# Optimization experiments

Measured on AMD Instinct MI355X. Metric: run time of the kernel, lower is better.

Reference implementation:

```python
import jax, jax.numpy as jnp
import numpy as np

B = 16384
D = 256        # feature_dim
EPS = 1e-5     # BatchNorm eps
NUM_CLASSES = 26

# cross-attention index pattern from the original double loop:
# for i in range(4): for j in range(4): if j != i: kv = features[4 - j - 1], q = features[i]
_Q_IDX = np.array([i for i in range(4) for j in range(4) if j != i])
_KV_IDX = np.array([3 - j for i in range(4) for j in range(4) if j != i])


def setup_inputs() -> dict:
    key = jax.random.key(0)
    ks = jax.random.split(key, 32)
    def n(k, shape, s=0.02):
        return jax.random.normal(k, shape, dtype=jnp.float32) * s
    inp = {
        'x_context': jax.random.normal(ks[0], (B, 2048), jnp.float32),
        'x_body':    jax.random.normal(ks[1], (B, 1024), jnp.float32),
        'x_face':    jax.random.normal(ks[2], (B, 512), jnp.float32),
        'x_text':    jax.random.normal(ks[3], (B, 768), jnp.float32),
        # modality input projections
        'w_ctx':  n(ks[4], (D, 2048)), 'b_ctx':  n(ks[5], (D,)),
        'w_body': n(ks[6], (D, 1024)), 'b_body': n(ks[7], (D,)),
        'w_face': n(ks[8], (D, 512)),  'b_face': n(ks[9], (D,)),
        'w_text': n(ks[10], (D, 768)), 'b_text': n(ks[11], (D,)),
        # shared nn.MultiheadAttention params (in_proj packs q,k,v)
        'in_proj_w': n(ks[12], (3 * D, D)), 'in_proj_b': n(ks[13], (3 * D,)),
        'out_w': n(ks[14], (D, D)), 'out_b': n(ks[15], (D,)),
        # gate MLP
        'gate_w1': n(ks[16], (D, D)), 'gate_b1': n(ks[17], (D,)),
        'gate_w2': n(ks[18], (1, D)), 'gate_b2': n(ks[19], (1,)),
        # head
        'fc1_w': n(ks[20], (D, D)), 'fc1_b': n(ks[21], (D,)),
        'bn_g': jnp.ones((D,), jnp.float32), 'bn_b': jnp.zeros((D,), jnp.float32),
        'fc2_w': n(ks[22], (NUM_CLASSES, D)), 'fc2_b': n(ks[23], (NUM_CLASSES,)),
    }
    return inp


def reference(x_context, x_body, x_face, x_text,
              w_ctx, b_ctx, w_body, b_body, w_face, b_face, w_text, b_text,
              in_proj_w, in_proj_b, out_w, out_b,
              gate_w1, gate_b1, gate_w2, gate_b2,
              fc1_w, fc1_b, bn_g, bn_b, fc2_w, fc2_b):
    # per-modality projections -> (4, B, D)
    f = jnp.stack([
        x_context @ w_ctx.T + b_ctx,
        x_body @ w_body.T + b_body,
        x_face @ w_face.T + b_face,
        x_text @ w_text.T + b_text,
    ], axis=0)

    # nn.MultiheadAttention with a single key/value token: softmax over one
    # logit is identically 1 (zero grad to q/k projections), so
    # attn(q, kv) = out_proj(v_proj(kv)) exactly.
    w_v = in_proj_w[2 * D:]
    b_v = in_proj_b[2 * D:]
    A = (f @ w_v.T + b_v) @ out_w.T + out_b            # (4, B, D)

    # self attention: attended_i + query_i, then mean over 4 modalities
    feats_self = jnp.mean(A + f, axis=0)               # (B, D)
    # cross attention: 12 (query, kv) pairs, then mean over 12
    feats_cross = jnp.mean(A[_KV_IDX] + f[_Q_IDX], axis=0)  # (B, D)

    gate = jax.nn.sigmoid(
        jax.nn.relu(feats_self @ gate_w1.T + gate_b1) @ gate_w2.T + gate_b2
    )                                                   # (B, 1)
    combined = gate * feats_self + (1.0 - gate) * feats_cross

    h = combined @ fc1_w.T + fc1_b
    # BatchNorm1d, training-mode batch statistics (biased var, as torch)
    mu = jnp.mean(h, axis=0)
    var = jnp.var(h, axis=0)
    h = (h - mu) * jax.lax.rsqrt(var + EPS) * bn_g + bn_b
    h = jax.nn.relu(h)
    # dropout omitted (deterministic reference)
    return h @ fc2_w.T + fc2_b                          # (B, 26)
```

## Files before the change

### kernel.cpp

```cpp
#include <hip/hip_runtime.h>
#include <hip/hip_bf16.h>
#include <stdint.h>

#define DM    256
#define KC    4352
#define NCLS  26

typedef __bf16 bf16;
typedef __attribute__((ext_vector_type(8))) __bf16 bf16x8;
typedef __attribute__((ext_vector_type(4))) __bf16 bf16x4;
typedef __attribute__((ext_vector_type(4))) float f32x4;
typedef __attribute__((ext_vector_type(4))) int i32x4;
typedef __attribute__((ext_vector_type(2))) int i32x2;

#define WQ_OFF    0u
#define SW_OFF    1114112u
#define COLF_OFF  1115136u
#define BSUM4_OFF 1116160u
#define CS_OFF    1117184u
#define CQ_OFF    1118208u
#define PTBF_OFF  1119232u
#define CC_OFF    1250304u
#define GT_OFF    1251328u
#define G_OFF     1382400u
#define FC2P_OFF  1383424u
#define FBAR_OFF  1400832u
#define H_OFF     9789440u

__device__ __forceinline__ bf16x8 cvt8(float4 a, float4 b) {
  bf16x8 r;
  r[0] = (bf16)a.x; r[1] = (bf16)a.y; r[2] = (bf16)a.z; r[3] = (bf16)a.w;
  r[4] = (bf16)b.x; r[5] = (bf16)b.y; r[6] = (bf16)b.z; r[7] = (bf16)b.w;
  return r;
}

__device__ __forceinline__ void gld_lds16(const void* g, void* l) {
  __builtin_amdgcn_global_load_lds(
      (const __attribute__((address_space(1))) void*)g,
      (__attribute__((address_space(3))) void*)l, 16, 0, 0);
}

__device__ __forceinline__ const float* pick(const float* x0, const float* x1,
                                             const float* x2, const float* x3,
                                             int k0, int& L, int& ko) {
  if (k0 < 2048)      { L = 2048; ko = k0;        return x0; }
  else if (k0 < 3072) { L = 1024; ko = k0 - 2048; return x1; }
  else if (k0 < 3584) { L = 512;  ko = k0 - 3072; return x2; }
  else                { L = 768;  ko = k0 - 3584; return x3; }
}

__device__ __forceinline__ int qpack4(float4 v, float s) {
  int a = (int)rintf(fminf(fmaxf(v.x * s, -127.f), 127.f));
  int b = (int)rintf(fminf(fmaxf(v.y * s, -127.f), 127.f));
  int c = (int)rintf(fminf(fmaxf(v.z * s, -127.f), 127.f));
  int d = (int)rintf(fminf(fmaxf(v.w * s, -127.f), 127.f));
  return (a & 255) | ((b & 255) << 8) | ((c & 255) << 16) | ((d & 255) << 24);
}

#define SXQ 25.4f

__global__ __launch_bounds__(256) void k_sw(
    const float* __restrict__ w0, const float* __restrict__ w1,
    const float* __restrict__ w2, const float* __restrict__ w3,
    float* __restrict__ sw) {
  __shared__ float red[4];
  int c = blockIdx.x, t = threadIdx.x;
  float m = 0.f;
  for (int k = t * 4; k < 2048; k += 1024) {
    float4 v = *(const float4*)(w0 + c * 2048 + k);
    m = fmaxf(m, fmaxf(fmaxf(fabsf(v.x), fabsf(v.y)), fmaxf(fabsf(v.z), fabsf(v.w))));
  }
  if (t * 4 < 1024) {
    float4 v = *(const float4*)(w1 + c * 1024 + t * 4);
    m = fmaxf(m, fmaxf(fmaxf(fabsf(v.x), fabsf(v.y)), fmaxf(fabsf(v.z), fabsf(v.w))));
  }
  if (t * 4 < 512) {
    float4 v = *(const float4*)(w2 + c * 512 + t * 4);
    m = fmaxf(m, fmaxf(fmaxf(fabsf(v.x), fabsf(v.y)), fmaxf(fabsf(v.z), fabsf(v.w))));
  }
  if (t * 4 < 768) {
    float4 v = *(const float4*)(w3 + c * 768 + t * 4);
    m = fmaxf(m, fmaxf(fmaxf(fabsf(v.x), fabsf(v.y)), fmaxf(fabsf(v.z), fabsf(v.w))));
  }
#pragma unroll
  for (int off = 32; off; off >>= 1) m = fmaxf(m, __shfl_xor(m, off));
  if ((t & 63) == 0) red[t >> 6] = m;
  __syncthreads();
  if (t == 0) sw[c] = fmaxf(fmaxf(red[0], red[1]), fmaxf(red[2], red[3]));
}

__global__ __launch_bounds__(256) void k_preA(
    const float* __restrict__ w0, const float* __restrict__ w1,
    const float* __restrict__ w2, const float* __restrict__ w3,
    const float* __restrict__ b0, const float* __restrict__ b1,
    const float* __restrict__ b2, const float* __restrict__ b3,
    const float* __restrict__ fc2_w, const float* __restrict__ sw,
    char* __restrict__ Wq, float* __restrict__ colf, float* __restrict__ bsum4,
    float* __restrict__ cs, float* __restrict__ cq, bf16* __restrict__ fc2p) {
  int bid = blockIdx.x;
  if (bid < 272) {
    int u = bid * 256 + threadIdx.x;
    int n16 = u / 4352;
    int rem = u % 4352;
    int kt = rem >> 6, lane = rem & 63;
    int col = n16 * 16 + (lane & 15);
    int k = kt * 64 + (lane >> 4) * 16;
    const float* src; int o;
    if (k < 2048)      { src = w0 + col * 2048; o = k; }
    else if (k < 3072) { src = w1 + col * 1024; o = k - 2048; }
    else if (k < 3584) { src = w2 + col * 512;  o = k - 3072; }
    else               { src = w3 + col * 768;  o = k - 3584; }
    float s = 127.f / sw[col];
    float4 a = *(const float4*)(src + o);
    float4 b = *(const float4*)(src + o + 4);
    float4 c = *(const float4*)(src + o + 8);
    float4 d = *(const float4*)(src + o + 12);
    i32x4 q;
    q[0] = qpack4(a, s); q[1] = qpack4(b, s); q[2] = qpack4(c, s); q[3] = qpack4(d, s);
    *(i32x4*)(Wq + (size_t)u * 16) = q;
  } else {
    int d = threadIdx.x;
    bsum4[d] = 0.25f * (b0[d] + b1[d] + b2[d] + b3[d]);
    colf[d] = 0.25f * (5.f / 127.f) * (sw[d] / 127.f);
    cs[d] = 0.f; cq[d] = 0.f;
#pragma unroll
    for (int rep = 0; rep < 4; ++rep) {
      int u2 = rep * 256 + threadIdx.x;
      int n16 = u2 >> 9, kf = (u2 >> 6) & 7, lane = u2 & 63;
      int row = n16 * 16 + (lane & 15);
      int kk = kf * 32 + (lane >> 4) * 8;
      bf16x8 v = {};
      if (row < 26) {
        float4 a = *(const float4*)(fc2_w + row * 256 + kk);
        float4 b = *(const float4*)(fc2_w + row * 256 + kk + 4);
        v = cvt8(a, b);
      }
      *(bf16x8*)(fc2p + (size_t)u2 * 8) = v;
    }
  }
}

__global__ __launch_bounds__(256) void k_preB(
    const float* __restrict__ in_proj_w, const float* __restrict__ in_proj_b,
    const float* __restrict__ out_w, const float* __restrict__ out_b,
    bf16* __restrict__ PTbf, float* __restrict__ cc) {
  int o0 = blockIdx.x * 16;
  int tid = threadIdx.x;
  int os = tid >> 6, iq = tid & 63;
  f32x4 facc[4] = {};
  float cacc[4] = {0.f, 0.f, 0.f, 0.f};
  for (int j = 0; j < 256; ++j) {
    f32x4 v = *(const f32x4*)(in_proj_w + (size_t)(512 + j) * 256 + iq * 4);
    float bv = in_proj_b[512 + j];
#pragma unroll
    for (int oo = 0; oo < 4; ++oo) {
      float w = out_w[(o0 + os * 4 + oo) * 256 + j];
      facc[oo] += v * w;
      cacc[oo] += bv * w;
    }
  }
#pragma unroll
  for (int oo = 0; oo < 4; ++oo) {
    int o = o0 + os * 4 + oo;
    bf16x4 r;
    r[0] = (bf16)facc[oo][0]; r[1] = (bf16)facc[oo][1];
    r[2] = (bf16)facc[oo][2]; r[3] = (bf16)facc[oo][3];
    *(bf16x4*)(PTbf + (size_t)o * 256 + iq * 4) = r;
    if (iq == 0) cc[o] = cacc[oo] + out_b[o];
  }
}

__global__ __launch_bounds__(256) void k_preC(
    const bf16* __restrict__ PTbf, const float* __restrict__ cc,
    const float* __restrict__ fc1_w, const float* __restrict__ fc1_b,
    bf16* __restrict__ GT, float* __restrict__ g) {
  __shared__ float fc1s[256];
  __shared__ float part[4][256];
  __shared__ float gbuf[256];
  int j = blockIdx.x;
  int tid = threadIdx.x;
  fc1s[tid] = fc1_w[j * 256 + tid];
  __syncthreads();
  int os = tid >> 6, lane = tid & 63;
  float a8[8] = {};
  for (int it = 0; it < 32; ++it) {
    int o = os * 64 + it * 2 + (lane >> 5);
    bf16x8 p = *(const bf16x8*)(PTbf + (size_t)o * 256 + (lane & 31) * 8);
    float w = fc1s[o];
#pragma unroll
    for (int e = 0; e < 8; ++e) a8[e] += (float)p[e] * w;
  }
#pragma unroll
  for (int e = 0; e < 8; ++e) a8[e] += __shfl_xor(a8[e], 32);
  if (lane < 32) {
#pragma unroll
    for (int e = 0; e < 8; ++e) part[os][(lane & 31) * 8 + e] = a8[e];
  }
  gbuf[tid] = cc[tid] * fc1s[tid];
  __syncthreads();
  int i = tid;
  float s = fc1s[i] + part[0][i] + part[1][i] + part[2][i] + part[3][i];
  int is = (i & ~63) | ((((i >> 3) & 7) ^ (j & 7)) << 3) | (i & 7);
  GT[j * 256 + is] = (bf16)s;
  if (tid == 0) {
    float t = 0.f;
    for (int o = 0; o < 256; ++o) t += gbuf[o];
    g[j] = t + fc1_b[j];
  }
}

__global__ __launch_bounds__(512, 2) void k_gemm1(
    const float* __restrict__ x0, const float* __restrict__ x1,
    const float* __restrict__ x2, const float* __restrict__ x3,
    const char* __restrict__ Wq, const float* __restrict__ colf,
    const float* __restrict__ bsum4, bf16* __restrict__ fbar) {
  __shared__ __align__(16) char ldsA[3][8192];
  int mt = blockIdx.x;
  int tid = threadIdx.x;
  int lane = tid & 63, wid = tid >> 6;
  int fr = lane & 15, fq = lane >> 4;
  i32x4 acc[4][2] = {};

  int arow = tid >> 3, achk = tid & 7;
  int wa = arow * 128 + (achk >> 2) * 64 + (((achk & 3) ^ (arow & 3)) << 4);
  const size_t xrow = (size_t)(mt * 64 + arow);
  const char* wq = Wq + (size_t)lane * 16;

  float4 arA[4], arB[4];
  i32x4 bbA[2][2], bbB[2][2];

  {
    int L, ko; const float* xs = pick(x0, x1, x2, x3, 0, L, ko);
    const float4* ap = (const float4*)(xs + xrow * L + ko) + achk * 4;
    float4 t0 = ap[0], t1 = ap[1], t2 = ap[2], t3 = ap[3];
#pragma unroll
    for (int n = 0; n < 2; ++n)
#pragma unroll
      for (int sb = 0; sb < 2; ++sb)
        bbA[n][sb] = *(const i32x4*)(wq + ((size_t)((2 * wid + n) * 68 + sb) << 10));
    xs = pick(x0, x1, x2, x3, 128, L, ko);
    ap = (const float4*)(xs + xrow * L + ko) + achk * 4;
    arB[0] = ap[0]; arB[1] = ap[1]; arB[2] = ap[2]; arB[3] = ap[3];
    i32x4 q;
    q[0] = qpack4(t0, SXQ); q[1] = qpack4(t1, SXQ);
    q[2] = qpack4(t2, SXQ); q[3] = qpack4(t3, SXQ);
    *(i32x4*)(&ldsA[0][wa]) = q;
    __builtin_amdgcn_sched_barrier(0);
    asm volatile("s_waitcnt lgkmcnt(0)" ::: "memory");
    __builtin_amdgcn_s_barrier();
    __builtin_amdgcn_sched_barrier(0);
  }

#define K1_BODY(S, BBU, BBL, ARU, ARL)                                         \
  do {                                                                         \
    int s1 = (s0 == 2) ? 0 : s0 + 1;                                           \
    if ((S) < 33) {                                                            \
      _Pragma("unroll") for (int n = 0; n < 2; ++n)                            \
      _Pragma("unroll") for (int sb = 0; sb < 2; ++sb)                         \
        BBL[n][sb] = *(const i32x4*)(wq +                                      \
            ((size_t)((2 * wid + n) * 68 + 2 * ((S) + 1) + sb) << 10));        \
    }                                                                          \
    if ((S) < 32) {                                                            \
      int L_, ko_;                                                             \
      const float* xs_ = pick(x0, x1, x2, x3, ((S) + 2) * 128, L_, ko_);       \
      const float4* ap_ = (const float4*)(xs_ + xrow * L_ + ko_) + achk * 4;   \
      ARL[0] = ap_[0]; ARL[1] = ap_[1]; ARL[2] = ap_[2]; ARL[3] = ap_[3];      \
    }                                                                          \
    if ((S) < 33) {                                                            \
      i32x4 q_;                                                                \
      q_[0] = qpack4(ARU[0], SXQ); q_[1] = qpack4(ARU[1], SXQ);                \
      q_[2] = qpack4(ARU[2], SXQ); q_[3] = qpack4(ARU[3], SXQ);                \
      *(i32x4*)(&ldsA[s1][wa]) = q_;                                           \
    }                                                                          \
    __builtin_amdgcn_sched_barrier(0);                                         \
    asm volatile("s_waitcnt lgkmcnt(0)" ::: "memory");                         \
    __builtin_amdgcn_s_barrier();                                              \
    __builtin_amdgcn_sched_barrier(0);                                         \
    const char* A_ = &ldsA[s0][0];                                             \
    i32x4 av[4][2];                                                            \
    _Pragma("unroll") for (int m = 0; m < 4; ++m) {                            \
      int row_ = m * 16 + fr;                                                  \
      _Pragma("unroll") for (int sb = 0; sb < 2; ++sb)                         \
        av[m][sb] = *(const i32x4*)(A_ + row_ * 128 + sb * 64 +                \
                                    ((fq ^ (row_ & 3)) << 4));                 \
    }                                                                          \
    __builtin_amdgcn_s_setprio(1);                                             \
    _Pragma("unroll") for (int sb = 0; sb < 2; ++sb)                           \
    _Pragma("unroll") for (int m = 0; m < 4; ++m)                              \
    _Pragma("unroll") for (int n = 0; n < 2; ++n)                              \
      acc[m][n] = __builtin_amdgcn_mfma_i32_16x16x64_i8(                       \
          av[m][sb], BBU[n][sb], acc[m][n], 0, 0, 0);                          \
    __builtin_amdgcn_s_setprio(0);                                             \
    s0 = s1;                                                                   \
  } while (0)

  int s0 = 0;
  for (int ss = 0; ss < 17; ++ss) {
    int S0 = ss * 2;
    K1_BODY(S0,     bbA, bbB, arB, arA);
    K1_BODY(S0 + 1, bbB, bbA, arA, arB);
  }
#undef K1_BODY

#pragma unroll
  for (int n = 0; n < 2; ++n) {
    int col = (2 * wid + n) * 16 + fr;
    float cf = colf[col];
    float b4 = bsum4[col];
#pragma unroll
    for (int m = 0; m < 4; ++m) {
      int row0 = mt * 64 + m * 16 + fq * 4;
#pragma unroll
      for (int r = 0; r < 4; ++r) {
        int row = row0 + r;
        int csw = (col & ~63) | ((((col >> 3) & 7) ^ (row & 7)) << 3) | (col & 7);
        fbar[(size_t)row * DM + csw] = (bf16)((float)acc[m][n][r] * cf + b4);
      }
    }
  }
}

__global__ __launch_bounds__(256, 4) void k_gemm2(
    const bf16* __restrict__ fbar, const bf16* __restrict__ GT,
    const float* __restrict__ g, bf16* __restrict__ h,
    float* __restrict__ cs, float* __restrict__ cq) {
  __shared__ __align__(16) bf16 lds[2][8192];
  int bid = blockIdx.x;
  int tile = (bid & 7) * 128 + (bid >> 3);
  int mt = tile >> 2, nt = tile & 3;
  int tid = threadIdx.x;
  int lane = tid & 63, wid = tid >> 6;
  int wr = wid >> 1, wc = wid & 1;
  int fr = lane & 15, fq = lane >> 4;
  f32x4 acc[2][2] = {};

  const size_t arow0 = (size_t)(mt * 64 + (tid >> 3)) * DM + (tid & 7) * 8;
  const size_t arow1 = (size_t)(mt * 64 + 32 + (tid >> 3)) * DM + (tid & 7) * 8;
  const size_t grow0 = (size_t)(nt * 64 + (tid >> 3)) * DM + (tid & 7) * 8;
  const size_t grow1 = (size_t)(nt * 64 + 32 + (tid >> 3)) * DM + (tid & 7) * 8;

  gld_lds16(fbar + arow0, &lds[0][tid * 8]);
  gld_lds16(fbar + arow1, &lds[0][2048 + tid * 8]);
  gld_lds16(GT + grow0, &lds[0][4096 + tid * 8]);
  gld_lds16(GT + grow1, &lds[0][4096 + 2048 + tid * 8]);
  __syncthreads();

  for (int kt = 0; kt < 4; ++kt) {
    int cur = kt & 1;
    if (kt < 3) {
      int k0 = (kt + 1) * 64;
      gld_lds16(fbar + arow0 + k0, &lds[cur ^ 1][tid * 8]);
      gld_lds16(fbar + arow1 + k0, &lds[cur ^ 1][2048 + tid * 8]);
      gld_lds16(GT + grow0 + k0, &lds[cur ^ 1][4096 + tid * 8]);
      gld_lds16(GT + grow1 + k0, &lds[cur ^ 1][4096 + 2048 + tid * 8]);
    }
    const bf16* A  = &lds[cur][0];
    const bf16* Bb = &lds[cur][4096];
    bf16x8 av[2][2], bv[2][2];
#pragma unroll
    for (int m = 0; m < 2; ++m) {
      int row = wr * 32 + m * 16 + fr;
#pragma unroll
      for (int kk = 0; kk < 2; ++kk)
        av[m][kk] = *(const bf16x8*)(A + row * 64 + ((((kk << 2) | fq) ^ (row & 7)) << 3));
    }
#pragma unroll
    for (int n = 0; n < 2; ++n) {
      int row = wc * 32 + n * 16 + fr;
#pragma unroll
      for (int kk = 0; kk < 2; ++kk)
        bv[n][kk] = *(const bf16x8*)(Bb + row * 64 + ((((kk << 2) | fq) ^ (row & 7)) << 3));
    }
#pragma unroll
    for (int kk = 0; kk < 2; ++kk)
#pragma unroll
      for (int m = 0; m < 2; ++m)
#pragma unroll
        for (int n = 0; n < 2; ++n)
          acc[m][n] = __builtin_amdgcn_mfma_f32_16x16x32_bf16(av[m][kk], bv[n][kk], acc[m][n], 0, 0, 0);
    __syncthreads();
  }

#pragma unroll
  for (int n = 0; n < 2; ++n) {
    int col = nt * 64 + wc * 32 + n * 16 + fr;
    float gv = g[col];
    float s = 0.f, q = 0.f;
#pragma unroll
    for (int m = 0; m < 2; ++m) {
      int row0 = mt * 64 + wr * 32 + m * 16 + fq * 4;
#pragma unroll
      for (int r = 0; r < 4; ++r) {
        float v = acc[m][n][r] + gv;
        h[(size_t)(row0 + r) * DM + col] = (bf16)v;
        s += v; q += v * v;
      }
    }
    s += __shfl_xor(s, 16); s += __shfl_xor(s, 32);
    q += __shfl_xor(q, 16); q += __shfl_xor(q, 32);
    if (fq == 0) { atomicAdd(&cs[col], s); atomicAdd(&cq[col], q); }
  }
}

__global__ __launch_bounds__(512) void k_fc2(
    const bf16* __restrict__ h, const float* __restrict__ cs, const float* __restrict__ cq,
    const float* __restrict__ bn_g, const float* __restrict__ bn_b,
    const bf16* __restrict__ fc2p, const float* __restrict__ fc2_b,
    float* __restrict__ out) {
  __shared__ float sdtd[512];
  int tid = threadIdx.x;
  int lane = tid & 63, wid = tid >> 6;
  int fr = lane & 15, fq = lane >> 4;
  if (tid < 256) {
    float mu = cs[tid] * (1.f / 16384.f);
    float var = cq[tid] * (1.f / 16384.f) - mu * mu;
    float s = bn_g[tid] * rsqrtf(var + 1e-5f);
    sdtd[tid] = s;
    sdtd[256 + tid] = bn_b[tid] - mu * s;
  }
  __syncthreads();
  int mtile = wid >> 1, n16 = wid & 1;
  int row0 = blockIdx.x * 64 + mtile * 16;
  f32x4 acc = {};
#pragma unroll
  for (int kf = 0; kf < 8; ++kf) {
    int c0 = kf * 32 + fq * 8;
    bf16x8 hv = *(const bf16x8*)(h + (size_t)(row0 + fr) * 256 + c0);
    bf16x8 y;
#pragma unroll
    for (int e = 0; e < 8; ++e) {
      float v = (float)hv[e] * sdtd[c0 + e] + sdtd[256 + c0 + e];
      y[e] = (bf16)fmaxf(v, 0.f);
    }
    bf16x8 bv = *(const bf16x8*)(fc2p + ((size_t)(n16 * 8 + kf) << 9) + lane * 8);
    acc = __builtin_amdgcn_mfma_f32_16x16x32_bf16(y, bv, acc, 0, 0, 0);
  }
  int col = n16 * 16 + fr;
  if (col < NCLS) {
    float bb = fc2_b[col];
#pragma unroll
    for (int r = 0; r < 4; ++r)
      out[(size_t)(row0 + fq * 4 + r) * NCLS + col] = acc[r] + bb;
  }
}

extern "C" void kernel_launch(void* const* d_in, const int* in_sizes, int n_in,
                              void* d_out, int out_size, void* d_ws, size_t ws_size,
                              hipStream_t stream) {
  (void)in_sizes; (void)n_in; (void)out_size; (void)ws_size;
  const float* x0 = (const float*)d_in[0];
  const float* x1 = (const float*)d_in[1];
  const float* x2 = (const float*)d_in[2];
  const float* x3 = (const float*)d_in[3];
  const float* w0 = (const float*)d_in[4];
  const float* b0 = (const float*)d_in[5];
  const float* w1 = (const float*)d_in[6];
  const float* b1 = (const float*)d_in[7];
  const float* w2 = (const float*)d_in[8];
  const float* b2 = (const float*)d_in[9];
  const float* w3 = (const float*)d_in[10];
  const float* b3 = (const float*)d_in[11];
  const float* in_proj_w = (const float*)d_in[12];
  const float* in_proj_b = (const float*)d_in[13];
  const float* out_w = (const float*)d_in[14];
  const float* out_b = (const float*)d_in[15];
  const float* fc1_w = (const float*)d_in[20];
  const float* fc1_b = (const float*)d_in[21];
  const float* bn_g = (const float*)d_in[22];
  const float* bn_b = (const float*)d_in[23];
  const float* fc2_w = (const float*)d_in[24];
  const float* fc2_b = (const float*)d_in[25];

  char* ws = (char*)d_ws;
  char* Wq    = ws + WQ_OFF;
  float* sw   = (float*)(ws + SW_OFF);
  float* colf = (float*)(ws + COLF_OFF);
  float* bsum4= (float*)(ws + BSUM4_OFF);
  float* cs   = (float*)(ws + CS_OFF);
  float* cq   = (float*)(ws + CQ_OFF);
  bf16* PTbf  = (bf16*)(ws + PTBF_OFF);
  float* cc   = (float*)(ws + CC_OFF);
  bf16* GT    = (bf16*)(ws + GT_OFF);
  float* g    = (float*)(ws + G_OFF);
  bf16* fc2p  = (bf16*)(ws + FC2P_OFF);
  bf16* fbar  = (bf16*)(ws + FBAR_OFF);
  bf16* h     = (bf16*)(ws + H_OFF);
  float* out  = (float*)d_out;

  k_sw<<<dim3(256), dim3(256), 0, stream>>>(w0, w1, w2, w3, sw);
  k_preA<<<dim3(273), dim3(256), 0, stream>>>(w0, w1, w2, w3, b0, b1, b2, b3,
                                              fc2_w, sw, Wq, colf, bsum4, cs, cq, fc2p);
  k_preB<<<dim3(16), dim3(256), 0, stream>>>(in_proj_w, in_proj_b, out_w, out_b, PTbf, cc);
  k_preC<<<dim3(256), dim3(256), 0, stream>>>(PTbf, cc, fc1_w, fc1_b, GT, g);
  k_gemm1<<<dim3(256), dim3(512), 0, stream>>>(x0, x1, x2, x3, Wq, colf, bsum4, fbar);
  k_gemm2<<<dim3(1024), dim3(256), 0, stream>>>(fbar, GT, g, h, cs, cq);
  k_fc2<<<dim3(256), dim3(512), 0, stream>>>(h, cs, cq, bn_g, bn_b, fc2p, fc2_b, out);
}
```

Baseline: 130.6 us.

## Fuse second GEMM into first GEMM epilogue and merge preB into sw kernel

The second GEMM (fbar times GT) now runs inside k_gemm1's epilogue. The fbar tile stays in LDS, and the B operand is read straight from a fragment-packed GT layout in global memory, so the fbar round-trip to HBM and the k_gemm2 launch both go away. The small preB weight-folding kernel is merged into the sw kernel as extra blocks, saving one more launch. The cost is 32KB more LDS per gemm1 block, which may cut occupancy, and each block now computes a full 64x256 tile on its own, so there is less parallelism than the old 1024-block gemm2.

```diff
diff --git a/kernel.cpp b/kernel.cpp
--- a/kernel.cpp
+++ b/kernel.cpp
@@ -11,7 +11,6 @@
 typedef __attribute__((ext_vector_type(4))) __bf16 bf16x4;
 typedef __attribute__((ext_vector_type(4))) float f32x4;
 typedef __attribute__((ext_vector_type(4))) int i32x4;
-typedef __attribute__((ext_vector_type(2))) int i32x2;
 
 #define WQ_OFF    0u
 #define SW_OFF    1114112u
@@ -24,20 +23,13 @@
 #define GT_OFF    1251328u
 #define G_OFF     1382400u
 #define FC2P_OFF  1383424u
-#define FBAR_OFF  1400832u
-#define H_OFF     9789440u
+#define H_OFF     1400832u
 
 __device__ __forceinline__ bf16x8 cvt8(float4 a, float4 b) {
   bf16x8 r;
   r[0] = (bf16)a.x; r[1] = (bf16)a.y; r[2] = (bf16)a.z; r[3] = (bf16)a.w;
   r[4] = (bf16)b.x; r[5] = (bf16)b.y; r[6] = (bf16)b.z; r[7] = (bf16)b.w;
   return r;
-}
-
-__device__ __forceinline__ void gld_lds16(const void* g, void* l) {
-  __builtin_amdgcn_global_load_lds(
-      (const __attribute__((address_space(1))) void*)g,
-      (__attribute__((address_space(3))) void*)l, 16, 0, 0);
 }
 
 __device__ __forceinline__ const float* pick(const float* x0, const float* x1,
@@ -59,34 +51,63 @@
 
 #define SXQ 25.4f
 
-__global__ __launch_bounds__(256) void k_sw(
+__global__ __launch_bounds__(256) void k_swB(
     const float* __restrict__ w0, const float* __restrict__ w1,
     const float* __restrict__ w2, const float* __restrict__ w3,
-    float* __restrict__ sw) {
-  __shared__ float red[4];
-  int c = blockIdx.x, t = threadIdx.x;
-  float m = 0.f;
-  for (int k = t * 4; k < 2048; k += 1024) {
-    float4 v = *(const float4*)(w0 + c * 2048 + k);
-    m = fmaxf(m, fmaxf(fmaxf(fabsf(v.x), fabsf(v.y)), fmaxf(fabsf(v.z), fabsf(v.w))));
-  }
-  if (t * 4 < 1024) {
-    float4 v = *(const float4*)(w1 + c * 1024 + t * 4);
-    m = fmaxf(m, fmaxf(fmaxf(fabsf(v.x), fabsf(v.y)), fmaxf(fabsf(v.z), fabsf(v.w))));
-  }
-  if (t * 4 < 512) {
-    float4 v = *(const float4*)(w2 + c * 512 + t * 4);
-    m = fmaxf(m, fmaxf(fmaxf(fabsf(v.x), fabsf(v.y)), fmaxf(fabsf(v.z), fabsf(v.w))));
-  }
-  if (t * 4 < 768) {
-    float4 v = *(const float4*)(w3 + c * 768 + t * 4);
-    m = fmaxf(m, fmaxf(fmaxf(fabsf(v.x), fabsf(v.y)), fmaxf(fabsf(v.z), fabsf(v.w))));
-  }
-#pragma unroll
-  for (int off = 32; off; off >>= 1) m = fmaxf(m, __shfl_xor(m, off));
-  if ((t & 63) == 0) red[t >> 6] = m;
-  __syncthreads();
-  if (t == 0) sw[c] = fmaxf(fmaxf(red[0], red[1]), fmaxf(red[2], red[3]));
+    const float* __restrict__ in_proj_w, const float* __restrict__ in_proj_b,
+    const float* __restrict__ out_w, const float* __restrict__ out_b,
+    float* __restrict__ sw, bf16* __restrict__ PTbf, float* __restrict__ cc) {
+  if (blockIdx.x < 256) {
+    __shared__ float red[4];
+    int c = blockIdx.x, t = threadIdx.x;
+    float m = 0.f;
+    for (int k = t * 4; k < 2048; k += 1024) {
+      float4 v = *(const float4*)(w0 + c * 2048 + k);
+      m = fmaxf(m, fmaxf(fmaxf(fabsf(v.x), fabsf(v.y)), fmaxf(fabsf(v.z), fabsf(v.w))));
+    }
+    if (t * 4 < 1024) {
+      float4 v = *(const float4*)(w1 + c * 1024 + t * 4);
+      m = fmaxf(m, fmaxf(fmaxf(fabsf(v.x), fabsf(v.y)), fmaxf(fabsf(v.z), fabsf(v.w))));
+    }
+    if (t * 4 < 512) {
+      float4 v = *(const float4*)(w2 + c * 512 + t * 4);
+      m = fmaxf(m, fmaxf(fmaxf(fabsf(v.x), fabsf(v.y)), fmaxf(fabsf(v.z), fabsf(v.w))));
+    }
+    if (t * 4 < 768) {
+      float4 v = *(const float4*)(w3 + c * 768 + t * 4);
+      m = fmaxf(m, fmaxf(fmaxf(fabsf(v.x), fabsf(v.y)), fmaxf(fabsf(v.z), fabsf(v.w))));
+    }
+#pragma unroll
+    for (int off = 32; off; off >>= 1) m = fmaxf(m, __shfl_xor(m, off));
+    if ((t & 63) == 0) red[t >> 6] = m;
+    __syncthreads();
+    if (t == 0) sw[c] = fmaxf(fmaxf(red[0], red[1]), fmaxf(red[2], red[3]));
+  } else {
+    int o0 = (blockIdx.x - 256) * 16;
+    int tid = threadIdx.x;
+    int os = tid >> 6, iq = tid & 63;
+    f32x4 facc[4] = {};
+    float cacc[4] = {0.f, 0.f, 0.f, 0.f};
+    for (int j = 0; j < 256; ++j) {
+      f32x4 v = *(const f32x4*)(in_proj_w + (size_t)(512 + j) * 256 + iq * 4);
+      float bv = in_proj_b[512 + j];
+#pragma unroll
+      for (int oo = 0; oo < 4; ++oo) {
+        float w = out_w[(o0 + os * 4 + oo) * 256 + j];
+        facc[oo] += v * w;
+        cacc[oo] += bv * w;
+      }
+    }
+#pragma unroll
+    for (int oo = 0; oo < 4; ++oo) {
+      int o = o0 + os * 4 + oo;
+      bf16x4 r;
+      r[0] = (bf16)facc[oo][0]; r[1] = (bf16)facc[oo][1];
+      r[2] = (bf16)facc[oo][2]; r[3] = (bf16)facc[oo][3];
+      *(bf16x4*)(PTbf + (size_t)o * 256 + iq * 4) = r;
+      if (iq == 0) cc[o] = cacc[oo] + out_b[o];
+    }
+  }
 }
 
 __global__ __launch_bounds__(256) void k_preA(
@@ -140,40 +161,10 @@
   }
 }
 
-__global__ __launch_bounds__(256) void k_preB(
-    const float* __restrict__ in_proj_w, const float* __restrict__ in_proj_b,
-    const float* __restrict__ out_w, const float* __restrict__ out_b,
-    bf16* __restrict__ PTbf, float* __restrict__ cc) {
-  int o0 = blockIdx.x * 16;
-  int tid = threadIdx.x;
-  int os = tid >> 6, iq = tid & 63;
-  f32x4 facc[4] = {};
-  float cacc[4] = {0.f, 0.f, 0.f, 0.f};
-  for (int j = 0; j < 256; ++j) {
-    f32x4 v = *(const f32x4*)(in_proj_w + (size_t)(512 + j) * 256 + iq * 4);
-    float bv = in_proj_b[512 + j];
-#pragma unroll
-    for (int oo = 0; oo < 4; ++oo) {
-      float w = out_w[(o0 + os * 4 + oo) * 256 + j];
-      facc[oo] += v * w;
-      cacc[oo] += bv * w;
-    }
-  }
-#pragma unroll
-  for (int oo = 0; oo < 4; ++oo) {
-    int o = o0 + os * 4 + oo;
-    bf16x4 r;
-    r[0] = (bf16)facc[oo][0]; r[1] = (bf16)facc[oo][1];
-    r[2] = (bf16)facc[oo][2]; r[3] = (bf16)facc[oo][3];
-    *(bf16x4*)(PTbf + (size_t)o * 256 + iq * 4) = r;
-    if (iq == 0) cc[o] = cacc[oo] + out_b[o];
-  }
-}
-
 __global__ __launch_bounds__(256) void k_preC(
     const bf16* __restrict__ PTbf, const float* __restrict__ cc,
     const float* __restrict__ fc1_w, const float* __restrict__ fc1_b,
-    bf16* __restrict__ GT, float* __restrict__ g) {
+    bf16* __restrict__ GTpack, float* __restrict__ g) {
   __shared__ float fc1s[256];
   __shared__ float part[4][256];
   __shared__ float gbuf[256];
@@ -200,8 +191,9 @@
   __syncthreads();
   int i = tid;
   float s = fc1s[i] + part[0][i] + part[1][i] + part[2][i] + part[3][i];
-  int is = (i & ~63) | ((((i >> 3) & 7) ^ (j & 7)) << 3) | (i & 7);
-  GT[j * 256 + is] = (bf16)s;
+  int unit = ((((j >> 4) * 4 + (i >> 6)) * 2 + ((i >> 5) & 1)) << 6)
+           + ((i >> 3) & 3) * 16 + (j & 15);
+  GTpack[(size_t)unit * 8 + (i & 7)] = (bf16)s;
   if (tid == 0) {
     float t = 0.f;
     for (int o = 0; o < 256; ++o) t += gbuf[o];
@@ -213,8 +205,11 @@
     const float* __restrict__ x0, const float* __restrict__ x1,
     const float* __restrict__ x2, const float* __restrict__ x3,
     const char* __restrict__ Wq, const float* __restrict__ colf,
-    const float* __restrict__ bsum4, bf16* __restrict__ fbar) {
+    const float* __restrict__ bsum4, const bf16* __restrict__ GTpack,
+    const float* __restrict__ g, bf16* __restrict__ h,
+    float* __restrict__ cs, float* __restrict__ cq) {
   __shared__ __align__(16) char ldsA[3][8192];
+  __shared__ __align__(16) bf16 ldsC[16384];
   int mt = blockIdx.x;
   int tid = threadIdx.x;
   int lane = tid & 63, wid = tid >> 6;
@@ -309,89 +304,60 @@
     float b4 = bsum4[col];
 #pragma unroll
     for (int m = 0; m < 4; ++m) {
-      int row0 = mt * 64 + m * 16 + fq * 4;
+      int row0l = m * 16 + fq * 4;
 #pragma unroll
       for (int r = 0; r < 4; ++r) {
-        int row = row0 + r;
+        int row = row0l + r;
         int csw = (col & ~63) | ((((col >> 3) & 7) ^ (row & 7)) << 3) | (col & 7);
-        fbar[(size_t)row * DM + csw] = (bf16)((float)acc[m][n][r] * cf + b4);
+        ldsC[row * 256 + csw] = (bf16)((float)acc[m][n][r] * cf + b4);
       }
     }
   }
-}
-
-__global__ __launch_bounds__(256, 4) void k_gemm2(
-    const bf16* __restrict__ fbar, const bf16* __restrict__ GT,
-    const float* __restrict__ g, bf16* __restrict__ h,
-    float* __restrict__ cs, float* __restrict__ cq) {
-  __shared__ __align__(16) bf16 lds[2][8192];
-  int bid = blockIdx.x;
-  int tile = (bid & 7) * 128 + (bid >> 3);
-  int mt = tile >> 2, nt = tile & 3;
-  int tid = threadIdx.x;
-  int lane = tid & 63, wid = tid >> 6;
-  int wr = wid >> 1, wc = wid & 1;
-  int fr = lane & 15, fq = lane >> 4;
-  f32x4 acc[2][2] = {};
-
-  const size_t arow0 = (size_t)(mt * 64 + (tid >> 3)) * DM + (tid & 7) * 8;
-  const size_t arow1 = (size_t)(mt * 64 + 32 + (tid >> 3)) * DM + (tid & 7) * 8;
-  const size_t grow0 = (size_t)(nt * 64 + (tid >> 3)) * DM + (tid & 7) * 8;
-  const size_t grow1 = (size_t)(nt * 64 + 32 + (tid >> 3)) * DM + (tid & 7) * 8;
-
-  gld_lds16(fbar + arow0, &lds[0][tid * 8]);
-  gld_lds16(fbar + arow1, &lds[0][2048 + tid * 8]);
-  gld_lds16(GT + grow0, &lds[0][4096 + tid * 8]);
-  gld_lds16(GT + grow1, &lds[0][4096 + 2048 + tid * 8]);
-  __syncthreads();
-
+  __builtin_amdgcn_sched_barrier(0);
+  asm volatile("s_waitcnt lgkmcnt(0)" ::: "memory");
+  __builtin_amdgcn_s_barrier();
+  __builtin_amdgcn_sched_barrier(0);
+
+  const bf16* gtp = GTpack + (size_t)lane * 8;
+  f32x4 acc2[4][2] = {};
+#pragma unroll
   for (int kt = 0; kt < 4; ++kt) {
-    int cur = kt & 1;
-    if (kt < 3) {
-      int k0 = (kt + 1) * 64;
-      gld_lds16(fbar + arow0 + k0, &lds[cur ^ 1][tid * 8]);
-      gld_lds16(fbar + arow1 + k0, &lds[cur ^ 1][2048 + tid * 8]);
-      gld_lds16(GT + grow0 + k0, &lds[cur ^ 1][4096 + tid * 8]);
-      gld_lds16(GT + grow1 + k0, &lds[cur ^ 1][4096 + 2048 + tid * 8]);
-    }
-    const bf16* A  = &lds[cur][0];
-    const bf16* Bb = &lds[cur][4096];
-    bf16x8 av[2][2], bv[2][2];
-#pragma unroll
-    for (int m = 0; m < 2; ++m) {
-      int row = wr * 32 + m * 16 + fr;
+    bf16x8 av2[4][2], bv2[2][2];
+#pragma unroll
+    for (int m = 0; m < 4; ++m) {
+      int row = m * 16 + fr;
 #pragma unroll
       for (int kk = 0; kk < 2; ++kk)
-        av[m][kk] = *(const bf16x8*)(A + row * 64 + ((((kk << 2) | fq) ^ (row & 7)) << 3));
-    }
-#pragma unroll
-    for (int n = 0; n < 2; ++n) {
-      int row = wc * 32 + n * 16 + fr;
+        av2[m][kk] = *(const bf16x8*)(ldsC + row * 256 + kt * 64 +
+                                      ((((kk << 2) | fq) ^ (row & 7)) << 3));
+    }
+#pragma unroll
+    for (int n = 0; n < 2; ++n)
 #pragma unroll
       for (int kk = 0; kk < 2; ++kk)
-        bv[n][kk] = *(const bf16x8*)(Bb + row * 64 + ((((kk << 2) | fq) ^ (row & 7)) << 3));
-    }
+        bv2[n][kk] = *(const bf16x8*)(gtp +
+            ((size_t)((2 * wid + n) * 8 + 2 * kt + kk) << 9));
 #pragma unroll
     for (int kk = 0; kk < 2; ++kk)
 #pragma unroll
-      for (int m = 0; m < 2; ++m)
+      for (int m = 0; m < 4; ++m)
 #pragma unroll
         for (int n = 0; n < 2; ++n)
-          acc[m][n] = __builtin_amdgcn_mfma_f32_16x16x32_bf16(av[m][kk], bv[n][kk], acc[m][n], 0, 0, 0);
-    __syncthreads();
+          acc2[m][n] = __builtin_amdgcn_mfma_f32_16x16x32_bf16(
+              av2[m][kk], bv2[n][kk], acc2[m][n], 0, 0, 0);
   }
 
 #pragma unroll
   for (int n = 0; n < 2; ++n) {
-    int col = nt * 64 + wc * 32 + n * 16 + fr;
+    int col = (2 * wid + n) * 16 + fr;
     float gv = g[col];
     float s = 0.f, q = 0.f;
 #pragma unroll
-    for (int m = 0; m < 2; ++m) {
-      int row0 = mt * 64 + wr * 32 + m * 16 + fq * 4;
+    for (int m = 0; m < 4; ++m) {
+      int row0 = mt * 64 + m * 16 + fq * 4;
 #pragma unroll
       for (int r = 0; r < 4; ++r) {
-        float v = acc[m][n][r] + gv;
+        float v = acc2[m][n][r] + gv;
         h[(size_t)(row0 + r) * DM + col] = (bf16)v;
         s += v; q += v * v;
       }
@@ -480,19 +446,19 @@
   float* cq   = (float*)(ws + CQ_OFF);
   bf16* PTbf  = (bf16*)(ws + PTBF_OFF);
   float* cc   = (float*)(ws + CC_OFF);
-  bf16* GT    = (bf16*)(ws + GT_OFF);
+  bf16* GTpk  = (bf16*)(ws + GT_OFF);
   float* g    = (float*)(ws + G_OFF);
   bf16* fc2p  = (bf16*)(ws + FC2P_OFF);
-  bf16* fbar  = (bf16*)(ws + FBAR_OFF);
   bf16* h     = (bf16*)(ws + H_OFF);
   float* out  = (float*)d_out;
 
-  k_sw<<<dim3(256), dim3(256), 0, stream>>>(w0, w1, w2, w3, sw);
+  k_swB<<<dim3(272), dim3(256), 0, stream>>>(w0, w1, w2, w3,
+                                             in_proj_w, in_proj_b, out_w, out_b,
+                                             sw, PTbf, cc);
   k_preA<<<dim3(273), dim3(256), 0, stream>>>(w0, w1, w2, w3, b0, b1, b2, b3,
                                               fc2_w, sw, Wq, colf, bsum4, cs, cq, fc2p);
-  k_preB<<<dim3(16), dim3(256), 0, stream>>>(in_proj_w, in_proj_b, out_w, out_b, PTbf, cc);
-  k_preC<<<dim3(256), dim3(256), 0, stream>>>(PTbf, cc, fc1_w, fc1_b, GT, g);
-  k_gemm1<<<dim3(256), dim3(512), 0, stream>>>(x0, x1, x2, x3, Wq, colf, bsum4, fbar);
-  k_gemm2<<<dim3(1024), dim3(256), 0, stream>>>(fbar, GT, g, h, cs, cq);
+  k_preC<<<dim3(256), dim3(256), 0, stream>>>(PTbf, cc, fc1_w, fc1_b, GTpk, g);
+  k_gemm1<<<dim3(256), dim3(512), 0, stream>>>(x0, x1, x2, x3, Wq, colf, bsum4,
+                                               GTpk, g, h, cs, cq);
   k_fc2<<<dim3(256), dim3(512), 0, stream>>>(h, cs, cq, bn_g, bn_b, fc2p, fc2_b, out);
 }
```

Result: faster. 108.6 us (-16.9%).
